# Kernel optimization log

Hardware: AMD Instinct MI355X
Metric: run time of the kernel (lower is better)

## Reference

```python
import jax, jax.numpy as jnp
import numpy as np
import math

N = 100000
E = 800000
H = 256
TDIM = 32
NTYPES = 22
NLAYERS = 2


def layer_norm(x, g, b, eps=1e-5):
    mu = jnp.mean(x, axis=-1, keepdims=True)
    var = jnp.var(x, axis=-1, keepdims=True)
    return (x - mu) * jax.lax.rsqrt(var + eps) * g + b


def setup_inputs() -> dict:
    key = jax.random.key(0)
    ks = jax.random.split(key, 16)
    s = 1.0 / math.sqrt(H)
    inp = {
        "clause_reprs": jax.random.normal(ks[0], (N, H), dtype=jnp.float32),
        "timestamps": jax.random.uniform(ks[1], (N,), dtype=jnp.float32) * 10000.0,
        "deriv_types": jax.random.randint(ks[2], (N,), 0, NTYPES),
        "derivation_edges": jax.random.randint(ks[3], (2, E), 0, N),
        # params
        "emb_table": jax.random.normal(ks[4], (NTYPES, H), dtype=jnp.float32),
        "temp_W": jax.random.normal(ks[5], (TDIM, H), dtype=jnp.float32) / math.sqrt(TDIM),
        "temp_b": jnp.zeros((H,), jnp.float32),
        "fus_W1": jax.random.normal(ks[6], (3 * H, H), dtype=jnp.float32) / math.sqrt(3 * H),
        "fus_b1": jnp.zeros((H,), jnp.float32),
        "fus_W2": jax.random.normal(ks[7], (H, H), dtype=jnp.float32) * s,
        "fus_b2": jnp.zeros((H,), jnp.float32),
        "in_g": jnp.ones((H,), jnp.float32),
        "in_b": jnp.zeros((H,), jnp.float32),
        "deriv_W": jax.random.normal(ks[8], (NLAYERS, 2 * H, H), dtype=jnp.float32) / math.sqrt(2 * H),
        "deriv_b": jnp.zeros((NLAYERS, H), jnp.float32),
        "dn_g": jnp.ones((NLAYERS, H), jnp.float32),
        "dn_b": jnp.zeros((NLAYERS, H), jnp.float32),
    }
    return inp


def reference(clause_reprs, timestamps, deriv_types, derivation_edges,
              emb_table, temp_W, temp_b, fus_W1, fus_b1, fus_W2, fus_b2,
              in_g, in_b, deriv_W, deriv_b, dn_g, dn_b):
    # --- temporal sinusoidal encoding -> projection ---
    half = TDIM // 2
    freqs = jnp.exp(-math.log(10000.0) * jnp.arange(half, dtype=jnp.float32) / half)
    angles = timestamps[:, None] * freqs[None, :]                      # (N, half)
    pe = jnp.concatenate([jnp.sin(angles), jnp.cos(angles)], axis=-1)  # (N, TDIM)
    temporal_enc = pe @ temp_W + temp_b                                # (N, H)
    # --- derivation type embedding ---
    deriv_enc = emb_table[deriv_types]                                 # (N, H)
    # --- input fusion + residual + LN ---
    cat = jnp.concatenate([clause_reprs, temporal_enc, deriv_enc], axis=-1)
    fused = jax.nn.relu(cat @ fus_W1 + fus_b1) @ fus_W2 + fus_b2
    x = layer_norm(fused + clause_reprs, in_g, in_b)
    # --- derivation message passing along DAG edges (parent -> child) ---
    src, dst = derivation_edges[0], derivation_edges[1]
    count = jnp.zeros((N, 1), jnp.float32).at[dst].add(1.0)
    count = jnp.maximum(count, 1.0)
    for l in range(NLAYERS):
        parent_msgs = x[src]                                           # (E, H) gather
        agg = jnp.zeros_like(x).at[dst].add(parent_msgs) / count       # (N, H) scatter-add
        combined = jnp.concatenate([x, agg], axis=-1)                  # (N, 2H)
        update = jax.nn.relu(combined @ deriv_W[l] + deriv_b[l])
        x = layer_norm(x + update, dn_g[l], dn_b[l])
    return x
```

## Files before the change

### kernel.cpp

```cpp
#include <hip/hip_runtime.h>
#include <hip/hip_bf16.h>
#include <math.h>

#define N_NODES 100000
#define N_EDGES 800000
#define H 256
#define NTYPES 22
#define SCAN_G 98
#define GRID5 ((N_NODES + 127) / 128)

typedef __attribute__((ext_vector_type(8))) short short8;
typedef __attribute__((ext_vector_type(4))) float f32x4;
typedef unsigned short u16;

__device__ __forceinline__ u16 f2bf(float f) {
    unsigned u = __float_as_uint(f);
    u += 0x7FFF + ((u >> 16) & 1);
    return (u16)(u >> 16);
}
__device__ __forceinline__ float bf2f(u16 u) {
    return __uint_as_float(((unsigned)u) << 16);
}
__device__ __forceinline__ int pi2(int k) {
    return (k & 192) | ((k & 3) << 4) | ((k >> 2) & 15);
}

__device__ __forceinline__ void gload16(const void* g, void* l) {
    __builtin_amdgcn_global_load_lds(
        (const __attribute__((address_space(1))) unsigned int*)g,
        (__attribute__((address_space(3))) unsigned int*)l, 16, 0, 0);
}

#define BAR_WAIT3()  do { __builtin_amdgcn_sched_barrier(0); \
    asm volatile("s_waitcnt vmcnt(3)\ns_barrier" ::: "memory"); } while (0)
#define BAR_WAIT2()  do { __builtin_amdgcn_sched_barrier(0); \
    asm volatile("s_waitcnt vmcnt(2)\ns_barrier" ::: "memory"); } while (0)
#define BAR_WAIT0()  do { __builtin_amdgcn_sched_barrier(0); \
    asm volatile("s_waitcnt vmcnt(0)\ns_barrier" ::: "memory"); } while (0)
#define BAR_WAIT0L() do { __builtin_amdgcn_sched_barrier(0); \
    asm volatile("s_waitcnt vmcnt(0) lgkmcnt(0)\ns_barrier" ::: "memory"); } while (0)
#define BAR_REL()    do { __builtin_amdgcn_sched_barrier(0); \
    asm volatile("s_barrier" ::: "memory"); } while (0)

__global__ __launch_bounds__(256) void conv_bf16(
    const float* __restrict__ src, u16* __restrict__ dst)
{
    size_t i = (size_t)blockIdx.x * 256 + threadIdx.x;
    const float4 a = ((const float4*)src)[i * 2];
    const float4 b = ((const float4*)src)[i * 2 + 1];
    short8 v;
    v[0] = (short)f2bf(a.x); v[1] = (short)f2bf(a.y);
    v[2] = (short)f2bf(a.z); v[3] = (short)f2bf(a.w);
    v[4] = (short)f2bf(b.x); v[5] = (short)f2bf(b.y);
    v[6] = (short)f2bf(b.z); v[7] = (short)f2bf(b.w);
    ((short8*)dst)[i] = v;
}

__global__ __launch_bounds__(256) void prep_small(
    const float* __restrict__ temp_W, const float* __restrict__ temp_b,
    const float* __restrict__ emb, const float* __restrict__ fus_W1,
    const float* __restrict__ fus_b1,
    float* __restrict__ C1, float* __restrict__ C2, float* __restrict__ beff)
{
    int b = blockIdx.x;
    int j = threadIdx.x;
    if (b < 32) {
        float acc = 0.f;
        #pragma unroll 8
        for (int m = 0; m < H; ++m)
            acc += temp_W[b * H + m] * fus_W1[(size_t)(H + m) * H + j];
        C1[b * H + j] = acc;
    } else if (b < 32 + NTYPES) {
        int e = b - 32;
        float acc = 0.f;
        #pragma unroll 8
        for (int m = 0; m < H; ++m)
            acc += emb[e * H + m] * fus_W1[(size_t)(2 * H + m) * H + j];
        C2[e * H + j] = acc;
    } else {
        float acc = fus_b1[j];
        #pragma unroll 8
        for (int m = 0; m < H; ++m)
            acc += temp_b[m] * fus_W1[(size_t)(H + m) * H + j];
        beff[j] = acc;
    }
}

__global__ __launch_bounds__(256) void prep_frag(
    const float* __restrict__ fus_W1, const float* __restrict__ C1,
    const float* __restrict__ fus_W2, const float* __restrict__ deriv_W,
    u16* __restrict__ wblob)
{
    int s = blockIdx.x;
    #pragma unroll
    for (int it = 0; it < 4; ++it) {
        int c = it * 256 + threadIdx.x;
        int l = c & 63, nt = c >> 6;
        int ncol = (nt << 4) | (l & 15);
        int kin = (l >> 4) << 3;
        short8 v;
        #pragma unroll
        for (int i = 0; i < 8; ++i) {
            const float* srcp;
            if (s < 8) {
                srcp = fus_W1 + (size_t)(s * 32 + kin + i) * H;
            } else if (s == 8) {
                srcp = C1 + (size_t)(kin + i) * H;
            } else if (s < 17) {
                int k = (s - 9) * 32 + kin + i;
                srcp = fus_W2 + (size_t)pi2(k) * H;
            } else if (s < 33) {
                int k = (s - 17) * 32 + kin + i;
                srcp = deriv_W + (size_t)((k >> 8) * 256 + pi2(k & 255)) * H;
            } else {
                int k = (s - 33) * 32 + kin + i;
                srcp = deriv_W + (size_t)(512 + (k >> 8) * 256 + pi2(k & 255)) * H;
            }
            v[i] = (short)f2bf(srcp[ncol]);
        }
        *reinterpret_cast<short8*>(wblob + (size_t)s * 8192 + (size_t)c * 8) = v;
    }
}

__global__ void count_kernel(const int* __restrict__ dst, int* __restrict__ cnt)
{
    int e = blockIdx.x * blockDim.x + threadIdx.x;
    if (e < N_EDGES) atomicAdd(&cnt[dst[e]], 1);
}

__global__ __launch_bounds__(1024) void scan1_kernel(
    const int* __restrict__ cnt, int* __restrict__ off, int* __restrict__ bsum)
{
    __shared__ int s[1024];
    int i = blockIdx.x * 1024 + threadIdx.x;
    int v = (i < N_NODES) ? cnt[i] : 0;
    s[threadIdx.x] = v;
    __syncthreads();
    #pragma unroll
    for (int o = 1; o < 1024; o <<= 1) {
        int t = (threadIdx.x >= o) ? s[threadIdx.x - o] : 0;
        __syncthreads();
        s[threadIdx.x] += t;
        __syncthreads();
    }
    if (i < N_NODES) off[i] = s[threadIdx.x];
    if (threadIdx.x == 1023) bsum[blockIdx.x] = s[1023];
}

__global__ void scan2_kernel(const int* __restrict__ bsum, int* __restrict__ bbase)
{
    if (threadIdx.x == 0) {
        int acc = 0;
        for (int b = 0; b < SCAN_G; ++b) { bbase[b] = acc; acc += bsum[b]; }
    }
}

__global__ __launch_bounds__(1024) void scan3_kernel(
    int* __restrict__ off, const int* __restrict__ bbase,
    const int* __restrict__ cnt, int* __restrict__ cursor)
{
    int i = blockIdx.x * 1024 + threadIdx.x;
    if (i < N_NODES) {
        int incl = off[i] + bbase[blockIdx.x];
        off[i] = incl;
        cursor[i] = incl - cnt[i];
    }
}

__global__ void fill_kernel(const int* __restrict__ src, const int* __restrict__ dst,
                            int* __restrict__ cursor, int* __restrict__ csr)
{
    int e = blockIdx.x * blockDim.x + threadIdx.x;
    if (e < N_EDGES) {
        int pos = atomicAdd(&cursor[dst[e]], 1);
        csr[pos] = src[e];
    }
}

__global__ __launch_bounds__(256) void gather_kernel(
    const u16* __restrict__ xb, const int* __restrict__ csr,
    const int* __restrict__ off, const int* __restrict__ cnt,
    u16* __restrict__ agg)
{
    int node = blockIdx.x * 4 + (threadIdx.x >> 6);
    int l = threadIdx.x & 63;
    int half = l >> 5, lc = l & 31;
    int deg = cnt[node];
    int start = off[node] - deg;
    float a[8] = {0.f, 0.f, 0.f, 0.f, 0.f, 0.f, 0.f, 0.f};
    int j = half;
    for (; j + 2 < deg; j += 4) {
        int s0 = csr[start + j];
        int s1 = csr[start + j + 2];
        short8 v0 = *reinterpret_cast<const short8*>(xb + (size_t)s0 * H + lc * 8);
        short8 v1 = *reinterpret_cast<const short8*>(xb + (size_t)s1 * H + lc * 8);
        #pragma unroll
        for (int i = 0; i < 8; ++i)
            a[i] += bf2f((u16)v0[i]) + bf2f((u16)v1[i]);
    }
    if (j < deg) {
        int s0 = csr[start + j];
        short8 v0 = *reinterpret_cast<const short8*>(xb + (size_t)s0 * H + lc * 8);
        #pragma unroll
        for (int i = 0; i < 8; ++i)
            a[i] += bf2f((u16)v0[i]);
    }
    #pragma unroll
    for (int i = 0; i < 8; ++i)
        a[i] += __shfl_xor(a[i], 32);
    if (half == 0) {
        float sc = 1.0f / fmaxf((float)deg, 1.0f);
        short8 o;
        #pragma unroll
        for (int i = 0; i < 8; ++i) o[i] = (short)f2bf(a[i] * sc);
        *reinterpret_cast<short8*>(agg + (size_t)node * H + lc * 8) = o;
    }
}

__device__ __forceinline__ void stageA8(u16* Af, const u16* __restrict__ src,
                                        int i0, int kbase, int tid)
{
    int rt = tid >> 6, l = tid & 63;
    int row = min(i0 + rt * 16 + (l & 15), N_NODES - 1);
    gload16(src + (size_t)row * H + kbase + ((l >> 4) << 3), Af + (tid << 3));
}

__device__ __forceinline__ void stageB8(u16* Bf, const u16* __restrict__ wk, int tid)
{
    gload16(wk + ((size_t)tid << 3),         Bf + (tid << 3));
    gload16(wk + ((size_t)(tid + 512) << 3), Bf + ((tid + 512) << 3));
}

__device__ __forceinline__ void mfma_step8(const u16* Af, const u16* Bf,
                                           int wm, int wn, int l, f32x4 acc[4][4])
{
    short8 a[4], b[4];
    #pragma unroll
    for (int m = 0; m < 4; ++m)
        a[m] = *reinterpret_cast<const short8*>(Af + ((((wm << 2) | m) << 6 | l) << 3));
    #pragma unroll
    for (int n = 0; n < 4; ++n)
        b[n] = *reinterpret_cast<const short8*>(Bf + ((((wn << 2) | n) << 6 | l) << 3));
    __builtin_amdgcn_s_setprio(1);
    #pragma unroll
    for (int n = 0; n < 4; ++n)
        #pragma unroll
        for (int m = 0; m < 4; ++m)
            acc[m][n] = __builtin_amdgcn_mfma_f32_16x16x32_bf16(a[m], b[n],
                                                                acc[m][n], 0, 0, 0);
    __builtin_amdgcn_s_setprio(0);
}

__global__ __launch_bounds__(512, 4) void k1_mfma(
    const u16* __restrict__ cb, const float* __restrict__ ts,
    const int* __restrict__ types, const u16* __restrict__ wblob,
    const float* __restrict__ C2, const float* __restrict__ beff,
    u16* __restrict__ hb)
{
    __shared__ __align__(16) u16 Af[2][4096];
    __shared__ __align__(16) u16 Bf[2][8192];
    int tid = threadIdx.x, w = tid >> 6, l = tid & 63;
    int wm = w >> 2, wn = w & 3, g = l >> 4, c0 = l & 15;
    int kg = g << 3;
    int i0 = blockIdx.x * 128;
    f32x4 acc[4][4] = {};

    short8 pv;
    {
        float tsv = ts[min(i0 + ((w << 4) | c0), N_NODES - 1)];
        #pragma unroll
        for (int i = 0; i < 8; ++i) {
            int k = kg + i;
            float fr = expf(-0.57564627324851f * (float)(k & 15));
            float ang = tsv * fr;
            pv[i] = (short)f2bf((k < 16) ? sinf(ang) : cosf(ang));
        }
    }

    stageA8(Af[0], cb, i0, 0, tid);
    stageB8(Bf[0], wblob, tid);
    #pragma unroll
    for (int t = 0; t < 9; ++t) {
        int cur = t & 1;
        if (t < 8) {
            if (t < 7) stageA8(Af[cur ^ 1], cb, i0, (t + 1) * 32, tid);
            stageB8(Bf[cur ^ 1], wblob + (size_t)(t + 1) * 8192, tid);
        }
        if (t == 8)
            *reinterpret_cast<short8*>(Af[0] + (tid << 3)) = pv;
        if (t < 7)       BAR_WAIT3();
        else if (t == 7) BAR_WAIT2();
        else             BAR_WAIT0L();
        mfma_step8(Af[cur], Bf[cur], wm, wn, l, acc);
        BAR_REL();
    }

    float bev[4];
    #pragma unroll
    for (int n = 0; n < 4; ++n) bev[n] = beff[(((wn << 2) | n) << 4) | c0];
    #pragma unroll
    for (int m = 0; m < 4; ++m) {
        #pragma unroll
        for (int r = 0; r < 4; ++r) {
            int rl = (((wm << 2) | m) << 4) + (g << 2) + r;
            int row = i0 + rl;
            bool ok = row < N_NODES;
            int tp = types[ok ? row : 0];
            const float* c2r = C2 + (size_t)tp * H;
            ushort4 o;
            float v0 = fmaxf(acc[m][0][r] + bev[0] + c2r[((wn << 2) << 4) | c0], 0.f);
            float v1 = fmaxf(acc[m][1][r] + bev[1] + c2r[(((wn << 2) | 1) << 4) | c0], 0.f);
            float v2 = fmaxf(acc[m][2][r] + bev[2] + c2r[(((wn << 2) | 2) << 4) | c0], 0.f);
            float v3 = fmaxf(acc[m][3][r] + bev[3] + c2r[(((wn << 2) | 3) << 4) | c0], 0.f);
            o.x = f2bf(v0); o.y = f2bf(v1); o.z = f2bf(v2); o.w = f2bf(v3);
            if (ok)
                *reinterpret_cast<ushort4*>(hb + (size_t)row * H + (wn << 6) + (c0 << 2)) = o;
        }
    }
}

__global__ __launch_bounds__(512, 4) void k2_mfma(
    const u16* __restrict__ hb, const u16* __restrict__ cb,
    const u16* __restrict__ wblob, const float* __restrict__ b2,
    const float* __restrict__ gW, const float* __restrict__ bW,
    u16* __restrict__ xb)
{
    __shared__ __align__(16) u16 Af[2][4096];
    __shared__ __align__(16) u16 Bf[2][8192];
    __shared__ float2 red[512];
    int tid = threadIdx.x, w = tid >> 6, l = tid & 63;
    int wm = w >> 2, wn = w & 3, g = l >> 4, c0 = l & 15;
    int i0 = blockIdx.x * 128;
    f32x4 acc[4][4] = {};

    stageA8(Af[0], hb, i0, 0, tid);
    stageB8(Bf[0], wblob, tid);
    #pragma unroll
    for (int t = 0; t < 8; ++t) {
        int cur = t & 1;
        if (t < 7) {
            stageA8(Af[cur ^ 1], hb, i0, (t + 1) * 32, tid);
            stageB8(Bf[cur ^ 1], wblob + (size_t)(t + 1) * 8192, tid);
        }
        if (t < 7) BAR_WAIT3(); else BAR_WAIT0();
        mfma_step8(Af[cur], Bf[cur], wm, wn, l, acc);
        BAR_REL();
    }

    float bv[4], gv[4], bbv[4];
    int lc[4];
    #pragma unroll
    for (int n = 0; n < 4; ++n) {
        lc[n] = (((wn << 2) | n) << 4) | c0;
        bv[n] = b2[lc[n]]; gv[n] = gW[lc[n]]; bbv[n] = bW[lc[n]];
    }
    #pragma unroll
    for (int m = 0; m < 4; ++m) {
        #pragma unroll
        for (int r = 0; r < 4; ++r) {
            int rl = (((wm << 2) | m) << 4) + (g << 2) + r;
            int rowc = min(i0 + rl, N_NODES - 1);
            const u16* cr = cb + (size_t)rowc * H;
            float s = 0.f, q = 0.f;
            #pragma unroll
            for (int n = 0; n < 4; ++n) {
                float pv = acc[m][n][r] + bv[n] + bf2f(cr[lc[n]]);
                acc[m][n][r] = pv;
                s += pv; q += pv * pv;
            }
            #pragma unroll
            for (int o = 1; o < 16; o <<= 1) {
                s += __shfl_xor(s, o);
                q += __shfl_xor(q, o);
            }
            if (c0 == 0) red[(rl << 2) | wn] = make_float2(s, q);
        }
    }
    __syncthreads();
    #pragma unroll
    for (int m = 0; m < 4; ++m) {
        #pragma unroll
        for (int r = 0; r < 4; ++r) {
            int rl = (((wm << 2) | m) << 4) + (g << 2) + r;
            int row = i0 + rl;
            float2 t0 = red[(rl << 2) | 0], t1 = red[(rl << 2) | 1];
            float2 t2 = red[(rl << 2) | 2], t3 = red[(rl << 2) | 3];
            float S = t0.x + t1.x + t2.x + t3.x;
            float Q = t0.y + t1.y + t2.y + t3.y;
            float mu = S * (1.0f / 256.0f);
            float rstd = rsqrtf(Q * (1.0f / 256.0f) - mu * mu + 1e-5f);
            if (row < N_NODES) {
                ushort4 o;
                o.x = f2bf((acc[m][0][r] - mu) * rstd * gv[0] + bbv[0]);
                o.y = f2bf((acc[m][1][r] - mu) * rstd * gv[1] + bbv[1]);
                o.z = f2bf((acc[m][2][r] - mu) * rstd * gv[2] + bbv[2]);
                o.w = f2bf((acc[m][3][r] - mu) * rstd * gv[3] + bbv[3]);
                *reinterpret_cast<ushort4*>(xb + (size_t)row * H + (wn << 6) + (c0 << 2)) = o;
            }
        }
    }
}

template<bool FINAL>
__global__ __launch_bounds__(512, 4) void k5_mfma(
    const u16* __restrict__ xb, const u16* __restrict__ aggb,
    const u16* __restrict__ wblob, const float* __restrict__ bl,
    const float* __restrict__ gl_, const float* __restrict__ bnl,
    u16* __restrict__ xbout, float* __restrict__ xout)
{
    __shared__ __align__(16) u16 Af[2][4096];
    __shared__ __align__(16) u16 Bf[2][8192];
    __shared__ float2 red[512];
    int tid = threadIdx.x, w = tid >> 6, l = tid & 63;
    int wm = w >> 2, wn = w & 3, g = l >> 4, c0 = l & 15;
    int i0 = blockIdx.x * 128;
    f32x4 acc[4][4] = {};

    stageA8(Af[0], xb, i0, 0, tid);
    stageB8(Bf[0], wblob, tid);
    #pragma unroll
    for (int t = 0; t < 16; ++t) {
        int cur = t & 1;
        if (t < 15) {
            int t1 = t + 1;
            stageA8(Af[cur ^ 1], (t1 < 8) ? xb : aggb, i0, (t1 & 7) * 32, tid);
            stageB8(Bf[cur ^ 1], wblob + (size_t)t1 * 8192, tid);
        }
        if (t < 15) BAR_WAIT3(); else BAR_WAIT0();
        mfma_step8(Af[cur], Bf[cur], wm, wn, l, acc);
        BAR_REL();
    }

    float bv[4], gv[4], bbv[4];
    int lc[4];
    #pragma unroll
    for (int n = 0; n < 4; ++n) {
        lc[n] = (((wn << 2) | n) << 4) | c0;
        bv[n] = bl[lc[n]]; gv[n] = gl_[lc[n]]; bbv[n] = bnl[lc[n]];
    }
    #pragma unroll
    for (int m = 0; m < 4; ++m) {
        #pragma unroll
        for (int r = 0; r < 4; ++r) {
            int rl = (((wm << 2) | m) << 4) + (g << 2) + r;
            int rowc = min(i0 + rl, N_NODES - 1);
            ushort4 xr = *reinterpret_cast<const ushort4*>(
                xb + (size_t)rowc * H + (wn << 6) + (c0 << 2));
            float p0 = bf2f(xr.x) + fmaxf(acc[m][0][r] + bv[0], 0.f);
            float p1 = bf2f(xr.y) + fmaxf(acc[m][1][r] + bv[1], 0.f);
            float p2 = bf2f(xr.z) + fmaxf(acc[m][2][r] + bv[2], 0.f);
            float p3 = bf2f(xr.w) + fmaxf(acc[m][3][r] + bv[3], 0.f);
            acc[m][0][r] = p0; acc[m][1][r] = p1;
            acc[m][2][r] = p2; acc[m][3][r] = p3;
            float s = p0 + p1 + p2 + p3;
            float q = p0 * p0 + p1 * p1 + p2 * p2 + p3 * p3;
            #pragma unroll
            for (int o = 1; o < 16; o <<= 1) {
                s += __shfl_xor(s, o);
                q += __shfl_xor(q, o);
            }
            if (c0 == 0) red[(rl << 2) | wn] = make_float2(s, q);
        }
    }
    __syncthreads();
    #pragma unroll
    for (int m = 0; m < 4; ++m) {
        #pragma unroll
        for (int r = 0; r < 4; ++r) {
            int rl = (((wm << 2) | m) << 4) + (g << 2) + r;
            int row = i0 + rl;
            float2 t0 = red[(rl << 2) | 0], t1 = red[(rl << 2) | 1];
            float2 t2 = red[(rl << 2) | 2], t3 = red[(rl << 2) | 3];
            float S = t0.x + t1.x + t2.x + t3.x;
            float Q = t0.y + t1.y + t2.y + t3.y;
            float mu = S * (1.0f / 256.0f);
            float rstd = rsqrtf(Q * (1.0f / 256.0f) - mu * mu + 1e-5f);
            if (row < N_NODES) {
                if (FINAL) {
                    #pragma unroll
                    for (int n = 0; n < 4; ++n)
                        xout[(size_t)row * H + lc[n]] =
                            (acc[m][n][r] - mu) * rstd * gv[n] + bbv[n];
                } else {
                    ushort4 o;
                    o.x = f2bf((acc[m][0][r] - mu) * rstd * gv[0] + bbv[0]);
                    o.y = f2bf((acc[m][1][r] - mu) * rstd * gv[1] + bbv[1]);
                    o.z = f2bf((acc[m][2][r] - mu) * rstd * gv[2] + bbv[2]);
                    o.w = f2bf((acc[m][3][r] - mu) * rstd * gv[3] + bbv[3]);
                    *reinterpret_cast<ushort4*>(
                        xbout + (size_t)row * H + (wn << 6) + (c0 << 2)) = o;
                }
            }
        }
    }
}

extern "C" void kernel_launch(void* const* d_in, const int* in_sizes, int n_in,
                              void* d_out, int out_size, void* d_ws, size_t ws_size,
                              hipStream_t stream)
{
    const float* clause  = (const float*)d_in[0];
    const float* ts      = (const float*)d_in[1];
    const int*   types   = (const int*)  d_in[2];
    const int*   edges   = (const int*)  d_in[3];
    const float* emb     = (const float*)d_in[4];
    const float* temp_W  = (const float*)d_in[5];
    const float* temp_b  = (const float*)d_in[6];
    const float* fus_W1  = (const float*)d_in[7];
    const float* fus_b1  = (const float*)d_in[8];
    const float* fus_W2  = (const float*)d_in[9];
    const float* fus_b2  = (const float*)d_in[10];
    const float* in_g    = (const float*)d_in[11];
    const float* in_b    = (const float*)d_in[12];
    const float* deriv_W = (const float*)d_in[13];
    const float* deriv_b = (const float*)d_in[14];
    const float* dn_g    = (const float*)d_in[15];
    const float* dn_b    = (const float*)d_in[16];

    char* p = (char*)d_ws;
    float* C1   = (float*)p;            p += 32 * H * 4;
    float* C2   = (float*)p;            p += NTYPES * H * 4;
    float* beff = (float*)p;            p += H * 4;
    int* cnt    = (int*)p;              p += N_NODES * 4;
    int* off    = (int*)p;              p += N_NODES * 4;
    int* cursor = (int*)p;              p += N_NODES * 4;
    int* bsum   = (int*)p;              p += 128 * 4;
    int* bbase  = (int*)p;              p += 128 * 4;
    int* csr    = (int*)p;              p += N_EDGES * 4;
    u16* wblob  = (u16*)p;              p += 49 * 8192 * 2;
    u16* B1     = (u16*)p;              p += (size_t)N_NODES * H * 2;
    u16* B2     = (u16*)p;              p += (size_t)N_NODES * H * 2;
    float* x    = (float*)d_out;

    const int* src = edges;
    const int* dst = edges + N_EDGES;

    conv_bf16<<<(N_NODES * H / 8 + 255) / 256, 256, 0, stream>>>(clause, B1);
    prep_small<<<32 + NTYPES + 1, 256, 0, stream>>>(temp_W, temp_b, emb, fus_W1,
                                                    fus_b1, C1, C2, beff);
    prep_frag<<<49, 256, 0, stream>>>(fus_W1, C1, fus_W2, deriv_W, wblob);

    hipMemsetAsync(cnt, 0, N_NODES * sizeof(int), stream);
    count_kernel<<<(N_EDGES + 255) / 256, 256, 0, stream>>>(dst, cnt);
    scan1_kernel<<<SCAN_G, 1024, 0, stream>>>(cnt, off, bsum);
    scan2_kernel<<<1, 64, 0, stream>>>(bsum, bbase);
    scan3_kernel<<<SCAN_G, 1024, 0, stream>>>(off, bbase, cnt, cursor);
    fill_kernel<<<(N_EDGES + 255) / 256, 256, 0, stream>>>(src, dst, cursor, csr);

    k1_mfma<<<GRID5, 512, 0, stream>>>(B1, ts, types, wblob, C2, beff, B2);
    k2_mfma<<<GRID5, 512, 0, stream>>>(B2, B1, wblob + (size_t)9 * 8192,
                                       fus_b2, in_g, in_b, B2);

    gather_kernel<<<N_NODES / 4, 256, 0, stream>>>(B2, csr, off, cnt, B1);
    k5_mfma<false><<<GRID5, 512, 0, stream>>>(
        B2, B1, wblob + (size_t)17 * 8192, deriv_b, dn_g, dn_b, B2, nullptr);
    gather_kernel<<<N_NODES / 4, 256, 0, stream>>>(B2, csr, off, cnt, B1);
    k5_mfma<true><<<GRID5, 512, 0, stream>>>(
        B2, B1, wblob + (size_t)33 * 8192, deriv_b + H, dn_g + H, dn_b + H,
        nullptr, x);
}
```

Baseline: 532.4 us.

## Store bf16 activations in column-plane layout and precompute positional encoding

All bf16 activation buffers switch from row-major [N,256] to four planes of [N,64] columns. Each GEMM A-tile load then reads a 128-byte contiguous row segment per row within one plane, instead of striding by 512 bytes. The sinusoidal encoding moves out of k1 into a separate kernel that writes a fifth plane, so k1 streams it like the other A tiles. This costs an extra launch and writes to the PE plane. Gather reads also switch to plane addressing, with each node's 512 bytes now split across four planes.

```diff
diff --git a/kernel.cpp b/kernel.cpp
--- a/kernel.cpp
+++ b/kernel.cpp
@@ -8,6 +8,7 @@
 #define NTYPES 22
 #define SCAN_G 98
 #define GRID5 ((N_NODES + 127) / 128)
+#define PS ((size_t)N_NODES * 64)
 
 typedef __attribute__((ext_vector_type(8))) short short8;
 typedef __attribute__((ext_vector_type(4))) float f32x4;
@@ -33,27 +34,57 @@
 
 #define BAR_WAIT3()  do { __builtin_amdgcn_sched_barrier(0); \
     asm volatile("s_waitcnt vmcnt(3)\ns_barrier" ::: "memory"); } while (0)
-#define BAR_WAIT2()  do { __builtin_amdgcn_sched_barrier(0); \
-    asm volatile("s_waitcnt vmcnt(2)\ns_barrier" ::: "memory"); } while (0)
 #define BAR_WAIT0()  do { __builtin_amdgcn_sched_barrier(0); \
     asm volatile("s_waitcnt vmcnt(0)\ns_barrier" ::: "memory"); } while (0)
-#define BAR_WAIT0L() do { __builtin_amdgcn_sched_barrier(0); \
-    asm volatile("s_waitcnt vmcnt(0) lgkmcnt(0)\ns_barrier" ::: "memory"); } while (0)
 #define BAR_REL()    do { __builtin_amdgcn_sched_barrier(0); \
     asm volatile("s_barrier" ::: "memory"); } while (0)
 
-__global__ __launch_bounds__(256) void conv_bf16(
-    const float* __restrict__ src, u16* __restrict__ dst)
-{
-    size_t i = (size_t)blockIdx.x * 256 + threadIdx.x;
-    const float4 a = ((const float4*)src)[i * 2];
-    const float4 b = ((const float4*)src)[i * 2 + 1];
-    short8 v;
-    v[0] = (short)f2bf(a.x); v[1] = (short)f2bf(a.y);
-    v[2] = (short)f2bf(a.z); v[3] = (short)f2bf(a.w);
-    v[4] = (short)f2bf(b.x); v[5] = (short)f2bf(b.y);
-    v[6] = (short)f2bf(b.z); v[7] = (short)f2bf(b.w);
-    ((short8*)dst)[i] = v;
+__global__ __launch_bounds__(256) void convT(
+    const float* __restrict__ src, u16* __restrict__ cbT)
+{
+    int row = blockIdx.x * 256 + threadIdx.x;
+    if (row >= N_NODES) return;
+    int plane = blockIdx.y;
+    const float* s = src + (size_t)row * H + plane * 64;
+    u16* d = cbT + (size_t)plane * PS + (size_t)row * 64;
+    #pragma unroll
+    for (int c = 0; c < 8; ++c) {
+        float4 a = *reinterpret_cast<const float4*>(s + c * 8);
+        float4 b = *reinterpret_cast<const float4*>(s + c * 8 + 4);
+        ushort4 o1, o2;
+        o1.x = f2bf(a.x); o1.y = f2bf(a.y); o1.z = f2bf(a.z); o1.w = f2bf(a.w);
+        o2.x = f2bf(b.x); o2.y = f2bf(b.y); o2.z = f2bf(b.z); o2.w = f2bf(b.w);
+        *reinterpret_cast<ushort4*>(d + c * 8) = o1;
+        *reinterpret_cast<ushort4*>(d + c * 8 + 4) = o2;
+    }
+}
+
+__global__ __launch_bounds__(256) void peT(
+    const float* __restrict__ ts, u16* __restrict__ dst)
+{
+    int row = blockIdx.x * 256 + threadIdx.x;
+    if (row >= N_NODES) return;
+    float tsv = ts[row];
+    u16 vals[32];
+    #pragma unroll
+    for (int f = 0; f < 16; ++f) {
+        float fr = expf(-0.57564627324851f * (float)f);
+        float ang = tsv * fr;
+        vals[f]      = f2bf(sinf(ang));
+        vals[f + 16] = f2bf(cosf(ang));
+    }
+    u16* d = dst + (size_t)row * 64;
+    #pragma unroll
+    for (int c = 0; c < 4; ++c) {
+        ushort4 o;
+        o.x = vals[c * 8 + 0]; o.y = vals[c * 8 + 1];
+        o.z = vals[c * 8 + 2]; o.w = vals[c * 8 + 3];
+        ushort4 p;
+        p.x = vals[c * 8 + 4]; p.y = vals[c * 8 + 5];
+        p.z = vals[c * 8 + 6]; p.w = vals[c * 8 + 7];
+        *reinterpret_cast<ushort4*>(d + c * 8) = o;
+        *reinterpret_cast<ushort4*>(d + c * 8 + 4) = p;
+    }
 }
 
 __global__ __launch_bounds__(256) void prep_small(
@@ -178,13 +209,14 @@
 }
 
 __global__ __launch_bounds__(256) void gather_kernel(
-    const u16* __restrict__ xb, const int* __restrict__ csr,
+    const u16* __restrict__ xbT, const int* __restrict__ csr,
     const int* __restrict__ off, const int* __restrict__ cnt,
-    u16* __restrict__ agg)
+    u16* __restrict__ aggT)
 {
     int node = blockIdx.x * 4 + (threadIdx.x >> 6);
     int l = threadIdx.x & 63;
     int half = l >> 5, lc = l & 31;
+    size_t lbase = (size_t)(lc >> 3) * PS + (lc & 7) * 8;
     int deg = cnt[node];
     int start = off[node] - deg;
     float a[8] = {0.f, 0.f, 0.f, 0.f, 0.f, 0.f, 0.f, 0.f};
@@ -192,15 +224,15 @@
     for (; j + 2 < deg; j += 4) {
         int s0 = csr[start + j];
         int s1 = csr[start + j + 2];
-        short8 v0 = *reinterpret_cast<const short8*>(xb + (size_t)s0 * H + lc * 8);
-        short8 v1 = *reinterpret_cast<const short8*>(xb + (size_t)s1 * H + lc * 8);
+        short8 v0 = *reinterpret_cast<const short8*>(xbT + lbase + (size_t)s0 * 64);
+        short8 v1 = *reinterpret_cast<const short8*>(xbT + lbase + (size_t)s1 * 64);
         #pragma unroll
         for (int i = 0; i < 8; ++i)
             a[i] += bf2f((u16)v0[i]) + bf2f((u16)v1[i]);
     }
     if (j < deg) {
         int s0 = csr[start + j];
-        short8 v0 = *reinterpret_cast<const short8*>(xb + (size_t)s0 * H + lc * 8);
+        short8 v0 = *reinterpret_cast<const short8*>(xbT + lbase + (size_t)s0 * 64);
         #pragma unroll
         for (int i = 0; i < 8; ++i)
             a[i] += bf2f((u16)v0[i]);
@@ -213,16 +245,16 @@
         short8 o;
         #pragma unroll
         for (int i = 0; i < 8; ++i) o[i] = (short)f2bf(a[i] * sc);
-        *reinterpret_cast<short8*>(agg + (size_t)node * H + lc * 8) = o;
-    }
-}
-
-__device__ __forceinline__ void stageA8(u16* Af, const u16* __restrict__ src,
-                                        int i0, int kbase, int tid)
+        *reinterpret_cast<short8*>(aggT + lbase + (size_t)node * 64) = o;
+    }
+}
+
+__device__ __forceinline__ void stageA8(u16* Af, const u16* __restrict__ plane,
+                                        int coff, int i0, int tid)
 {
     int rt = tid >> 6, l = tid & 63;
     int row = min(i0 + rt * 16 + (l & 15), N_NODES - 1);
-    gload16(src + (size_t)row * H + kbase + ((l >> 4) << 3), Af + (tid << 3));
+    gload16(plane + (size_t)row * 64 + coff + ((l >> 4) << 3), Af + (tid << 3));
 }
 
 __device__ __forceinline__ void stageB8(u16* Bf, const u16* __restrict__ wk, int tid)
@@ -252,45 +284,31 @@
 }
 
 __global__ __launch_bounds__(512, 4) void k1_mfma(
-    const u16* __restrict__ cb, const float* __restrict__ ts,
-    const int* __restrict__ types, const u16* __restrict__ wblob,
-    const float* __restrict__ C2, const float* __restrict__ beff,
-    u16* __restrict__ hb)
+    const u16* __restrict__ cbT, const u16* __restrict__ wblob,
+    const int* __restrict__ types, const float* __restrict__ C2,
+    const float* __restrict__ beff, u16* __restrict__ hbT)
 {
     __shared__ __align__(16) u16 Af[2][4096];
     __shared__ __align__(16) u16 Bf[2][8192];
     int tid = threadIdx.x, w = tid >> 6, l = tid & 63;
     int wm = w >> 2, wn = w & 3, g = l >> 4, c0 = l & 15;
-    int kg = g << 3;
     int i0 = blockIdx.x * 128;
     f32x4 acc[4][4] = {};
 
-    short8 pv;
-    {
-        float tsv = ts[min(i0 + ((w << 4) | c0), N_NODES - 1)];
-        #pragma unroll
-        for (int i = 0; i < 8; ++i) {
-            int k = kg + i;
-            float fr = expf(-0.57564627324851f * (float)(k & 15));
-            float ang = tsv * fr;
-            pv[i] = (short)f2bf((k < 16) ? sinf(ang) : cosf(ang));
-        }
-    }
-
-    stageA8(Af[0], cb, i0, 0, tid);
+    stageA8(Af[0], cbT, 0, i0, tid);
     stageB8(Bf[0], wblob, tid);
     #pragma unroll
     for (int t = 0; t < 9; ++t) {
         int cur = t & 1;
         if (t < 8) {
-            if (t < 7) stageA8(Af[cur ^ 1], cb, i0, (t + 1) * 32, tid);
-            stageB8(Bf[cur ^ 1], wblob + (size_t)(t + 1) * 8192, tid);
-        }
-        if (t == 8)
-            *reinterpret_cast<short8*>(Af[0] + (tid << 3)) = pv;
-        if (t < 7)       BAR_WAIT3();
-        else if (t == 7) BAR_WAIT2();
-        else             BAR_WAIT0L();
+            int t1 = t + 1;
+            const u16* pl = (t1 < 8) ? cbT + (size_t)(t1 >> 1) * PS
+                                     : cbT + (size_t)4 * PS;
+            int coff = (t1 < 8) ? (t1 & 1) * 32 : 0;
+            stageA8(Af[cur ^ 1], pl, coff, i0, tid);
+            stageB8(Bf[cur ^ 1], wblob + (size_t)t1 * 8192, tid);
+        }
+        if (t < 8) BAR_WAIT3(); else BAR_WAIT0();
         mfma_step8(Af[cur], Bf[cur], wm, wn, l, acc);
         BAR_REL();
     }
@@ -314,16 +332,17 @@
             float v3 = fmaxf(acc[m][3][r] + bev[3] + c2r[(((wn << 2) | 3) << 4) | c0], 0.f);
             o.x = f2bf(v0); o.y = f2bf(v1); o.z = f2bf(v2); o.w = f2bf(v3);
             if (ok)
-                *reinterpret_cast<ushort4*>(hb + (size_t)row * H + (wn << 6) + (c0 << 2)) = o;
+                *reinterpret_cast<ushort4*>(
+                    hbT + (size_t)wn * PS + (size_t)row * 64 + (c0 << 2)) = o;
         }
     }
 }
 
 __global__ __launch_bounds__(512, 4) void k2_mfma(
-    const u16* __restrict__ hb, const u16* __restrict__ cb,
+    const u16* __restrict__ hbT, const u16* __restrict__ cbT,
     const u16* __restrict__ wblob, const float* __restrict__ b2,
     const float* __restrict__ gW, const float* __restrict__ bW,
-    u16* __restrict__ xb)
+    u16* __restrict__ xbT)
 {
     __shared__ __align__(16) u16 Af[2][4096];
     __shared__ __align__(16) u16 Bf[2][8192];
@@ -333,14 +352,15 @@
     int i0 = blockIdx.x * 128;
     f32x4 acc[4][4] = {};
 
-    stageA8(Af[0], hb, i0, 0, tid);
+    stageA8(Af[0], hbT, 0, i0, tid);
     stageB8(Bf[0], wblob, tid);
     #pragma unroll
     for (int t = 0; t < 8; ++t) {
         int cur = t & 1;
         if (t < 7) {
-            stageA8(Af[cur ^ 1], hb, i0, (t + 1) * 32, tid);
-            stageB8(Bf[cur ^ 1], wblob + (size_t)(t + 1) * 8192, tid);
+            int t1 = t + 1;
+            stageA8(Af[cur ^ 1], hbT + (size_t)(t1 >> 1) * PS, (t1 & 1) * 32, i0, tid);
+            stageB8(Bf[cur ^ 1], wblob + (size_t)t1 * 8192, tid);
         }
         if (t < 7) BAR_WAIT3(); else BAR_WAIT0();
         mfma_step8(Af[cur], Bf[cur], wm, wn, l, acc);
@@ -360,11 +380,11 @@
         for (int r = 0; r < 4; ++r) {
             int rl = (((wm << 2) | m) << 4) + (g << 2) + r;
             int rowc = min(i0 + rl, N_NODES - 1);
-            const u16* cr = cb + (size_t)rowc * H;
             float s = 0.f, q = 0.f;
             #pragma unroll
             for (int n = 0; n < 4; ++n) {
-                float pv = acc[m][n][r] + bv[n] + bf2f(cr[lc[n]]);
+                u16 cv = cbT[(size_t)(lc[n] >> 6) * PS + (size_t)rowc * 64 + (lc[n] & 63)];
+                float pv = acc[m][n][r] + bv[n] + bf2f(cv);
                 acc[m][n][r] = pv;
                 s += pv; q += pv * pv;
             }
@@ -395,7 +415,8 @@
                 o.y = f2bf((acc[m][1][r] - mu) * rstd * gv[1] + bbv[1]);
                 o.z = f2bf((acc[m][2][r] - mu) * rstd * gv[2] + bbv[2]);
                 o.w = f2bf((acc[m][3][r] - mu) * rstd * gv[3] + bbv[3]);
-                *reinterpret_cast<ushort4*>(xb + (size_t)row * H + (wn << 6) + (c0 << 2)) = o;
+                *reinterpret_cast<ushort4*>(
+                    xbT + (size_t)wn * PS + (size_t)row * 64 + (c0 << 2)) = o;
             }
         }
     }
@@ -403,7 +424,7 @@
 
 template<bool FINAL>
 __global__ __launch_bounds__(512, 4) void k5_mfma(
-    const u16* __restrict__ xb, const u16* __restrict__ aggb,
+    const u16* __restrict__ xbT, const u16* __restrict__ aggT,
     const u16* __restrict__ wblob, const float* __restrict__ bl,
     const float* __restrict__ gl_, const float* __restrict__ bnl,
     u16* __restrict__ xbout, float* __restrict__ xout)
@@ -416,14 +437,16 @@
     int i0 = blockIdx.x * 128;
     f32x4 acc[4][4] = {};
 
-    stageA8(Af[0], xb, i0, 0, tid);
+    stageA8(Af[0], xbT, 0, i0, tid);
     stageB8(Bf[0], wblob, tid);
     #pragma unroll
     for (int t = 0; t < 16; ++t) {
         int cur = t & 1;
         if (t < 15) {
             int t1 = t + 1;
-            stageA8(Af[cur ^ 1], (t1 < 8) ? xb : aggb, i0, (t1 & 7) * 32, tid);
+            const u16* pl = (t1 < 8) ? xbT + (size_t)(t1 >> 1) * PS
+                                     : aggT + (size_t)((t1 - 8) >> 1) * PS;
+            stageA8(Af[cur ^ 1], pl, (t1 & 1) * 32, i0, tid);
             stageB8(Bf[cur ^ 1], wblob + (size_t)t1 * 8192, tid);
         }
         if (t < 15) BAR_WAIT3(); else BAR_WAIT0();
@@ -445,7 +468,7 @@
             int rl = (((wm << 2) | m) << 4) + (g << 2) + r;
             int rowc = min(i0 + rl, N_NODES - 1);
             ushort4 xr = *reinterpret_cast<const ushort4*>(
-                xb + (size_t)rowc * H + (wn << 6) + (c0 << 2));
+                xbT + (size_t)wn * PS + (size_t)rowc * 64 + (c0 << 2));
             float p0 = bf2f(xr.x) + fmaxf(acc[m][0][r] + bv[0], 0.f);
             float p1 = bf2f(xr.y) + fmaxf(acc[m][1][r] + bv[1], 0.f);
             float p2 = bf2f(xr.z) + fmaxf(acc[m][2][r] + bv[2], 0.f);
@@ -488,7 +511,7 @@
                     o.z = f2bf((acc[m][2][r] - mu) * rstd * gv[2] + bbv[2]);
                     o.w = f2bf((acc[m][3][r] - mu) * rstd * gv[3] + bbv[3]);
                     *reinterpret_cast<ushort4*>(
-                        xbout + (size_t)row * H + (wn << 6) + (c0 << 2)) = o;
+                        xbout + (size_t)wn * PS + (size_t)row * 64 + (c0 << 2)) = o;
                 }
             }
         }
@@ -528,14 +551,16 @@
     int* bbase  = (int*)p;              p += 128 * 4;
     int* csr    = (int*)p;              p += N_EDGES * 4;
     u16* wblob  = (u16*)p;              p += 49 * 8192 * 2;
-    u16* B1     = (u16*)p;              p += (size_t)N_NODES * H * 2;
-    u16* B2     = (u16*)p;              p += (size_t)N_NODES * H * 2;
+    u16* cbT    = (u16*)p;              p += 5 * PS * 2;
+    u16* B2T    = (u16*)p;              p += 4 * PS * 2;
+    u16* aggT   = cbT;
     float* x    = (float*)d_out;
 
     const int* src = edges;
     const int* dst = edges + N_EDGES;
 
-    conv_bf16<<<(N_NODES * H / 8 + 255) / 256, 256, 0, stream>>>(clause, B1);
+    convT<<<dim3((N_NODES + 255) / 256, 4), 256, 0, stream>>>(clause, cbT);
+    peT<<<(N_NODES + 255) / 256, 256, 0, stream>>>(ts, cbT + (size_t)4 * PS);
     prep_small<<<32 + NTYPES + 1, 256, 0, stream>>>(temp_W, temp_b, emb, fus_W1,
                                                     fus_b1, C1, C2, beff);
     prep_frag<<<49, 256, 0, stream>>>(fus_W1, C1, fus_W2, deriv_W, wblob);
@@ -547,15 +572,15 @@
     scan3_kernel<<<SCAN_G, 1024, 0, stream>>>(off, bbase, cnt, cursor);
     fill_kernel<<<(N_EDGES + 255) / 256, 256, 0, stream>>>(src, dst, cursor, csr);
 
-    k1_mfma<<<GRID5, 512, 0, stream>>>(B1, ts, types, wblob, C2, beff, B2);
-    k2_mfma<<<GRID5, 512, 0, stream>>>(B2, B1, wblob + (size_t)9 * 8192,
-                                       fus_b2, in_g, in_b, B2);
-
-    gather_kernel<<<N_NODES / 4, 256, 0, stream>>>(B2, csr, off, cnt, B1);
+    k1_mfma<<<GRID5, 512, 0, stream>>>(cbT, wblob, types, C2, beff, B2T);
+    k2_mfma<<<GRID5, 512, 0, stream>>>(B2T, cbT, wblob + (size_t)9 * 8192,
+                                       fus_b2, in_g, in_b, B2T);
+
+    gather_kernel<<<N_NODES / 4, 256, 0, stream>>>(B2T, csr, off, cnt, aggT);
     k5_mfma<false><<<GRID5, 512, 0, stream>>>(
-        B2, B1, wblob + (size_t)17 * 8192, deriv_b, dn_g, dn_b, B2, nullptr);
-    gather_kernel<<<N_NODES / 4, 256, 0, stream>>>(B2, csr, off, cnt, B1);
+        B2T, aggT, wblob + (size_t)17 * 8192, deriv_b, dn_g, dn_b, B2T, nullptr);
+    gather_kernel<<<N_NODES / 4, 256, 0, stream>>>(B2T, csr, off, cnt, aggT);
     k5_mfma<true><<<GRID5, 512, 0, stream>>>(
-        B2, B1, wblob + (size_t)33 * 8192, deriv_b + H, dn_g + H, dn_b + H,
+        B2T, aggT, wblob + (size_t)33 * 8192, deriv_b + H, dn_g + H, dn_b + H,
         nullptr, x);
 }
```

Measured after the change: 588.3 us. 10.5% more time.
